# Performance work log

Measured on AMD Instinct MI355X. Metric: run time of the kernel, lower is better.

## Reference

```python
import jax, jax.numpy as jnp
import numpy as np

B, N, C = 32, 512, 256          # batch, proposals per scene, pooled feature dim
K = 16                          # knn neighbors
NN = B * N                      # total nodes = 16384
E = NN * K                      # total edges = 262144
L0_IN = 2 * C + 7               # EdgeConv layer-0 input (edge embedding appended)
EPS = 1e-5


def _xavier(key, fan_in, fan_out):
    s = float(np.sqrt(6.0 / (fan_in + fan_out)))
    return jax.random.uniform(key, (fan_in, fan_out), jnp.float32, -s, s)


def setup_inputs() -> dict:
    key = jax.random.key(0)
    ks = jax.random.split(key, 12)
    inp = {}
    inp["pooled_features"] = jax.random.normal(ks[0], (B, N, C), jnp.float32)
    inp["rois"] = jax.random.normal(ks[1], (B, N, 7), jnp.float32)
    inp["edge_src"] = jax.random.randint(ks[2], (E,), 0, NN)
    inp["edge_dst"] = jax.random.randint(ks[3], (E,), 0, NN)
    # global-info MLP: Linear(C+7 -> C) + BatchNorm(C) + ReLU
    inp["Wg"] = _xavier(ks[4], C + 7, C)
    inp["bg"] = jnp.zeros((C,), jnp.float32)
    inp["gg"] = jnp.ones((C,), jnp.float32)
    inp["betag"] = jnp.zeros((C,), jnp.float32)
    # EdgeConv 0: Linear(2C+7 -> C); EdgeConv 1,2: Linear(2C -> C)
    inp["W0"] = _xavier(ks[5], L0_IN, C)
    inp["b0"] = jnp.zeros((C,), jnp.float32)
    inp["g0"] = jnp.ones((C,), jnp.float32)
    inp["beta0"] = jnp.zeros((C,), jnp.float32)
    inp["W1"] = _xavier(ks[6], 2 * C, C)
    inp["b1"] = jnp.zeros((C,), jnp.float32)
    inp["g1"] = jnp.ones((C,), jnp.float32)
    inp["beta1"] = jnp.zeros((C,), jnp.float32)
    inp["W2"] = _xavier(ks[7], 2 * C, C)
    inp["b2"] = jnp.zeros((C,), jnp.float32)
    inp["g2"] = jnp.ones((C,), jnp.float32)
    inp["beta2"] = jnp.zeros((C,), jnp.float32)
    return inp


def _bn_relu(h, gamma, beta):
    # training-mode BatchNorm over the row (node/edge) dimension
    mu = jnp.mean(h, axis=0)
    var = jnp.mean(jnp.square(h - mu), axis=0)
    return jax.nn.relu((h - mu) * jax.lax.rsqrt(var + EPS) * gamma + beta)


def _edge_conv(x, src, dst, edge_attr, W, b, gamma, beta):
    x_j = x[src]          # source-node features  [E, D]
    x_i = x[dst]          # target-node features  [E, D]
    parts = [x_j - x_i, x_i]
    if edge_attr is not None:
        parts.append(edge_attr)
    m = jnp.concatenate(parts, axis=-1)          # [E, in_dim]
    h = _bn_relu(m @ W + b, gamma, beta)         # [E, C]
    out = jax.ops.segment_max(h, dst, num_segments=NN)  # scatter-max per target node
    return jnp.where(jnp.isneginf(out), 0.0, out)        # empty segments -> 0


def reference(pooled_features, rois, edge_src, edge_dst,
              Wg, bg, gg, betag,
              W0, b0, g0, beta0,
              W1, b1, g1, beta1,
              W2, b2, g2, beta2):
    boxes = rois.reshape(NN, 7)
    pf = pooled_features.reshape(NN, C)
    # global information MLP (CONCATENATED): cat(pooled, boxes) -> Linear+BN+ReLU
    x0 = _bn_relu(jnp.concatenate([pf, boxes], axis=-1) @ Wg + bg, gg, betag)
    # edge embedding: box delta from source to target
    edge_attr = boxes[edge_src] - boxes[edge_dst]
    x1 = _edge_conv(x0, edge_src, edge_dst, edge_attr, W0, b0, g0, beta0)
    x2 = _edge_conv(x1, edge_src, edge_dst, None, W1, b1, g1, beta1)
    x3 = _edge_conv(x2, edge_src, edge_dst, None, W2, b2, g2, beta2)
    return jnp.concatenate([x0, x1, x2, x3], axis=-1)  # related_features [NN, 4C]
```

## Files before the change

### kernel.cpp

```cpp
#include <hip/hip_runtime.h>
#include <hip/hip_bf16.h>
#include <hip/hip_fp16.h>
#include <math.h>
#include <stdint.h>


constexpr int NNODE = 16384;
constexpr int NEDGE = 262144;
constexpr int CD    = 256;
constexpr float EPSB = 1e-5f;

typedef __attribute__((ext_vector_type(8))) short bf16x8;
typedef __attribute__((ext_vector_type(8))) unsigned short u16x8;
typedef __attribute__((ext_vector_type(4))) float f32x4;
typedef __attribute__((ext_vector_type(4))) _Float16 h16x4;
typedef __attribute__((ext_vector_type(8))) _Float16 h16x8;

__device__ inline unsigned short bf_hi_rne(float f) {
  unsigned int u = __float_as_uint(f);
  u += 0x7fffu + ((u >> 16) & 1u);
  return (unsigned short)(u >> 16);
}

__global__ void build_wt(const float* __restrict__ W, const float* __restrict__ b,
                         unsigned short* __restrict__ Wth, unsigned short* __restrict__ Wtl,
                         int has_box) {
  int k = threadIdx.x;
  int n = blockIdx.x;
  if (k >= 288) return;
  float v = 0.0f;
  if (n < 256) {
    if (k < 256)      v = W[k * 256 + n];
    else if (k < 263) v = has_box ? W[(512 + (k - 256)) * 256 + n] : 0.0f;
  } else {
    int n2 = n - 256;
    if (k < 256)      v = W[(256 + k) * 256 + n2] - W[k * 256 + n2];
    else if (k < 263) v = has_box ? -W[(512 + (k - 256)) * 256 + n2] : 0.0f;
    else if (k == 263) v = b[n2];
  }
  unsigned short hi = bf_hi_rne(v);
  float fh = __uint_as_float((unsigned int)hi << 16);
  Wth[n * 288 + k] = hi;
  Wtl[n * 288 + k] = bf_hi_rne(v - fh);
}

__global__ void build_wtg(const float* __restrict__ Wg, const float* __restrict__ bg,
                          unsigned short* __restrict__ Wth, unsigned short* __restrict__ Wtl) {
  int k = threadIdx.x;
  int n = blockIdx.x;
  if (k >= 288) return;
  float v = 0.0f;
  if (k < 263)       v = Wg[k * 256 + n];
  else if (k == 263) v = bg[n];
  unsigned short hi = bf_hi_rne(v);
  float fh = __uint_as_float((unsigned int)hi << 16);
  Wth[n * 288 + k] = hi;
  Wtl[n * 288 + k] = bf_hi_rne(v - fh);
}

__global__ void build_boxf(const float* __restrict__ rois, float* __restrict__ boxf) {
  int n = blockIdx.x * 256 + threadIdx.x;
  float v[8];
#pragma unroll
  for (int j = 0; j < 7; j++) v[j] = rois[n * 7 + j];
  v[7] = 1.0f;
  *(float4*)(boxf + (size_t)n * 8)     = make_float4(v[0], v[1], v[2], v[3]);
  *(float4*)(boxf + (size_t)n * 8 + 4) = make_float4(v[4], v[5], v[6], v[7]);
}

__global__ void hist_kernel(const int* __restrict__ dst, int* __restrict__ counts) {
  int e = blockIdx.x * 256 + threadIdx.x;
  atomicAdd(&counts[dst[e]], 1);
}

__global__ __launch_bounds__(1024) void scan_kernel(const int* __restrict__ counts,
                                                    int* __restrict__ offsets,
                                                    int* __restrict__ cursor) {
  __shared__ int ssum[1024];
  int t = threadIdx.x;
  int base = t * 16;
  int loc[16];
  int s = 0;
#pragma unroll
  for (int i = 0; i < 16; i++) { loc[i] = s; s += counts[base + i]; }
  ssum[t] = s;
  __syncthreads();
  for (int off = 1; off < 1024; off <<= 1) {
    int v = (t >= off) ? ssum[t - off] : 0;
    __syncthreads();
    ssum[t] += v;
    __syncthreads();
  }
  int excl = (t > 0) ? ssum[t - 1] : 0;
#pragma unroll
  for (int i = 0; i < 16; i++) {
    int o = excl + loc[i];
    offsets[base + i] = o;
    cursor[base + i]  = o;
  }
  if (t == 1023) offsets[NNODE] = excl + s;
}

__global__ void scatter_kernel(const int* __restrict__ src, const int* __restrict__ dst,
                               int* __restrict__ cursor, int* __restrict__ csr_src) {
  int e = blockIdx.x * 256 + threadIdx.x;
  int p = atomicAdd(&cursor[dst[e]], 1);
  csr_src[p] = src[e];
}

__global__ __launch_bounds__(256) void gemm_mfma(
    const float* __restrict__ X, int xstride,
    const float* __restrict__ boxf,
    const unsigned short* __restrict__ Wth, const unsigned short* __restrict__ Wtl,
    float* __restrict__ out, int Nw, int half_out) {
  __shared__ alignas(16) char lds[4 * 8192];
  const int tid  = threadIdx.x;
  const int lane = tid & 63;
  const int wave = tid >> 6;
  const int wm = wave >> 1, wn = wave & 1;
  const int m0 = blockIdx.x * 128;
  const int n0 = blockIdx.y * 128;
  const int srow0 = tid >> 2;
  const int sc8   = tid & 3;

  f32x4 acc[4][4];
#pragma unroll
  for (int i = 0; i < 4; i++)
#pragma unroll
    for (int j = 0; j < 4; j++) acc[i][j] = (f32x4)0.0f;

  float a_f[2][8];
  u16x8 b_h[2], b_l[2];

  auto load_global = [&](int kt) {
#pragma unroll
    for (int p = 0; p < 2; p++) {
      int row = p * 64 + srow0;
      if (kt < 8) {
        const float* src = X + (size_t)(m0 + row) * xstride + kt * 32 + sc8 * 8;
        float4 v0 = *(const float4*)src;
        float4 v1 = *(const float4*)(src + 4);
        a_f[p][0] = v0.x; a_f[p][1] = v0.y; a_f[p][2] = v0.z; a_f[p][3] = v0.w;
        a_f[p][4] = v1.x; a_f[p][5] = v1.y; a_f[p][6] = v1.z; a_f[p][7] = v1.w;
      } else if (sc8 == 0) {
        float4 v0 = *(const float4*)(boxf + (size_t)(m0 + row) * 8);
        float4 v1 = *(const float4*)(boxf + (size_t)(m0 + row) * 8 + 4);
        a_f[p][0] = v0.x; a_f[p][1] = v0.y; a_f[p][2] = v0.z; a_f[p][3] = v0.w;
        a_f[p][4] = v1.x; a_f[p][5] = v1.y; a_f[p][6] = v1.z; a_f[p][7] = v1.w;
      } else {
#pragma unroll
        for (int j = 0; j < 8; j++) a_f[p][j] = 0.0f;
      }
      const size_t woff = (size_t)(n0 + row) * 288 + kt * 32 + sc8 * 8;
      b_h[p] = *(const u16x8*)(Wth + woff);
      b_l[p] = *(const u16x8*)(Wtl + woff);
    }
  };

  auto write_lds = [&]() {
#pragma unroll
    for (int p = 0; p < 2; p++) {
      int row = p * 64 + srow0;
      int off = row * 64 + 16 * sc8;
      u16x8 hi, lo;
#pragma unroll
      for (int j = 0; j < 8; j++) {
        float f = a_f[p][j];
        unsigned short h = bf_hi_rne(f);
        float fh = __uint_as_float((unsigned int)h << 16);
        hi[j] = h;
        lo[j] = bf_hi_rne(f - fh);
      }
      *(u16x8*)(lds + off)         = hi;
      *(u16x8*)(lds + 8192 + off)  = lo;
      *(u16x8*)(lds + 16384 + off) = b_h[p];
      *(u16x8*)(lds + 24576 + off) = b_l[p];
    }
  };

  load_global(0);
  const int kblk = lane >> 4;
  for (int kt = 0; kt < 9; kt++) {
    __syncthreads();
    write_lds();
    __syncthreads();
    if (kt < 8) load_global(kt + 1);

    bf16x8 ah[4], al[4];
#pragma unroll
    for (int i = 0; i < 4; i++) {
      int fm = wm * 64 + i * 16 + (lane & 15);
      int off = fm * 64 + 16 * kblk;
      ah[i] = *(const bf16x8*)(lds + off);
      al[i] = *(const bf16x8*)(lds + 8192 + off);
    }
#pragma unroll
    for (int j = 0; j < 4; j++) {
      int fn = wn * 64 + j * 16 + (lane & 15);
      int off = fn * 64 + 16 * kblk;
      bf16x8 bh = *(const bf16x8*)(lds + 16384 + off);
      bf16x8 bl = *(const bf16x8*)(lds + 24576 + off);
#pragma unroll
      for (int i = 0; i < 4; i++) {
        acc[i][j] = __builtin_amdgcn_mfma_f32_16x16x32_bf16(bh, ah[i], acc[i][j], 0, 0, 0);
        acc[i][j] = __builtin_amdgcn_mfma_f32_16x16x32_bf16(bh, al[i], acc[i][j], 0, 0, 0);
        acc[i][j] = __builtin_amdgcn_mfma_f32_16x16x32_bf16(bl, ah[i], acc[i][j], 0, 0, 0);
      }
    }
  }
#pragma unroll
  for (int i = 0; i < 4; i++) {
    int m = m0 + wm * 64 + i * 16 + (lane & 15);
#pragma unroll
    for (int j = 0; j < 4; j++) {
      int n = n0 + wn * 64 + j * 16 + (lane >> 4) * 4;
      if (half_out) {
        h16x4 o;
        o[0] = (_Float16)acc[i][j].x; o[1] = (_Float16)acc[i][j].y;
        o[2] = (_Float16)acc[i][j].z; o[3] = (_Float16)acc[i][j].w;
        *(h16x4*)((_Float16*)out + (size_t)m * Nw + n) = o;
      } else {
        *(f32x4*)(out + (size_t)m * Nw + n) = acc[i][j];
      }
    }
  }
}

constexpr int EPB = 8;
__global__ __launch_bounds__(256) void edge_pass(
    const _Float16* __restrict__ PQ,
    const int* __restrict__ offsets, const int* __restrict__ csr_src,
    float* __restrict__ M, float* __restrict__ psum, float* __restrict__ psq) {
  __shared__ float red[2][4][256];
  const int tid = threadIdx.x;
  const int wave = tid >> 6, lane = tid & 63;
  const int h = lane >> 5, li = lane & 31;
  const int c8 = li * 8;
  float sum[8] = {}, sq[8] = {};

  for (int nn = 0; nn < 2; nn++) {
    const int d = blockIdx.x * EPB + wave * 2 + nn;
    const int beg = offsets[d], end = offsets[d + 1];
    if (beg >= end) continue;
    h16x8 qv = *(const h16x8*)(PQ + (size_t)d * 512 + 256 + c8);
    float qf[8], mx[8];
#pragma unroll
    for (int j = 0; j < 8; j++) { qf[j] = (float)qv[j]; mx[j] = -INFINITY; }

    for (int e = beg; e < end; e += 8) {
      int idx[4];
      bool full = (e + 8 <= end);
      if (full) {
#pragma unroll
        for (int i = 0; i < 4; i++) idx[i] = csr_src[e + 2 * i + h];
        h16x8 pv[4];
#pragma unroll
        for (int i = 0; i < 4; i++)
          pv[i] = *(const h16x8*)(PQ + (size_t)idx[i] * 512 + c8);
#pragma unroll
        for (int i = 0; i < 4; i++)
#pragma unroll
          for (int j = 0; j < 8; j++) {
            float hh = (float)pv[i][j] + qf[j];
            mx[j] = fmaxf(mx[j], hh);
            sum[j] += hh;
            sq[j] = fmaf(hh, hh, sq[j]);
          }
      } else {
        bool live[4];
#pragma unroll
        for (int i = 0; i < 4; i++) {
          int ei = e + 2 * i + h;
          live[i] = ei < end;
          idx[i] = csr_src[live[i] ? ei : end - 1];
        }
        h16x8 pv[4];
#pragma unroll
        for (int i = 0; i < 4; i++)
          pv[i] = *(const h16x8*)(PQ + (size_t)idx[i] * 512 + c8);
#pragma unroll
        for (int i = 0; i < 4; i++)
#pragma unroll
          for (int j = 0; j < 8; j++) {
            float hh = (float)pv[i][j] + qf[j];
            mx[j] = fmaxf(mx[j], hh);
            float z = live[i] ? hh : 0.0f;
            sum[j] += z;
            sq[j] = fmaf(z, z, sq[j]);
          }
      }
    }
#pragma unroll
    for (int j = 0; j < 8; j++)
      mx[j] = fmaxf(mx[j], __shfl_xor(mx[j], 32));
    float4 o = (h == 0) ? make_float4(mx[0], mx[1], mx[2], mx[3])
                        : make_float4(mx[4], mx[5], mx[6], mx[7]);
    *(float4*)(M + (size_t)d * 256 + c8 + h * 4) = o;
  }

#pragma unroll
  for (int j = 0; j < 8; j++) {
    sum[j] += __shfl_xor(sum[j], 32);
    sq[j]  += __shfl_xor(sq[j], 32);
  }
  if (h == 0) {
    float4 s0 = make_float4(sum[0], sum[1], sum[2], sum[3]);
    float4 s1 = make_float4(sum[4], sum[5], sum[6], sum[7]);
    float4 q0 = make_float4(sq[0], sq[1], sq[2], sq[3]);
    float4 q1 = make_float4(sq[4], sq[5], sq[6], sq[7]);
    *(float4*)&red[0][wave][c8]     = s0;
    *(float4*)&red[0][wave][c8 + 4] = s1;
    *(float4*)&red[1][wave][c8]     = q0;
    *(float4*)&red[1][wave][c8 + 4] = q1;
  }
  __syncthreads();
  int c = tid;
  float ts = red[0][0][c] + red[0][1][c] + red[0][2][c] + red[0][3][c];
  float tq = red[1][0][c] + red[1][1][c] + red[1][2][c] + red[1][3][c];
  atomicAdd(&psum[c], ts);
  atomicAdd(&psq[c], tq);
}

__global__ void stats_dense(const float* __restrict__ H,
                            float* __restrict__ psum, float* __restrict__ psq) {
  int c  = threadIdx.x;
  int r0 = blockIdx.x * 16;
  float sum = 0.f, sq = 0.f;
  for (int r = r0; r < r0 + 16; r++) {
    float h = H[r * CD + c];
    sum += h;
    sq  += h * h;
  }
  atomicAdd(&psum[c], sum);
  atomicAdd(&psq[c], sq);
}

__global__ void finalize_stats(const float* __restrict__ psum, const float* __restrict__ psq,
                               float invcount, float* __restrict__ mu, float* __restrict__ rstd) {
  int c = threadIdx.x;
  float m = psum[c] * invcount;
  float v = psq[c] * invcount - m * m;
  v = fmaxf(v, 0.0f);
  mu[c]   = m;
  rstd[c] = 1.0f / sqrtf(v + EPSB);
}

__global__ void normalize_write(const float* __restrict__ H, const int* __restrict__ counts,
                                const float* __restrict__ mu, const float* __restrict__ rstd,
                                const float* __restrict__ gamma, const float* __restrict__ beta,
                                float* __restrict__ out, int col0) {
  int c  = threadIdx.x;
  int n0 = blockIdx.x * 8;
  float mc = mu[c], rc = rstd[c], gc = gamma[c], bc = beta[c];
  for (int n = n0; n < n0 + 8; n++) {
    float v = 0.0f;
    if (!counts || counts[n] != 0) {
      float h = H[n * CD + c];
      v = fmaxf((h - mc) * rc * gc + bc, 0.0f);
    }
    out[n * 1024 + col0 + c] = v;
  }
}

extern "C" void kernel_launch(void* const* d_in, const int* in_sizes, int n_in,
                              void* d_out, int out_size, void* d_ws, size_t ws_size,
                              hipStream_t stream) {
  const float* pf    = (const float*)d_in[0];
  const float* rois  = (const float*)d_in[1];
  const int*   esrc  = (const int*)d_in[2];
  const int*   edst  = (const int*)d_in[3];
  const float* Wg    = (const float*)d_in[4];
  const float* bg    = (const float*)d_in[5];
  const float* gg    = (const float*)d_in[6];
  const float* betag = (const float*)d_in[7];
  const float* Wl[3]  = {(const float*)d_in[8],  (const float*)d_in[12], (const float*)d_in[16]};
  const float* bl[3]  = {(const float*)d_in[9],  (const float*)d_in[13], (const float*)d_in[17]};
  const float* gl[3]  = {(const float*)d_in[10], (const float*)d_in[14], (const float*)d_in[18]};
  const float* bel[3] = {(const float*)d_in[11], (const float*)d_in[15], (const float*)d_in[19]};
  float* out = (float*)d_out;

  float* ws    = (float*)d_ws;
  _Float16* PQ = (_Float16*)ws;
  float* Mbuf  = ws + (size_t)NNODE * 256;
  float* psum  = Mbuf + (size_t)NNODE * CD;
  float* psq   = psum + CD;
  float* mu    = psq + CD;
  float* rstd  = mu + CD;
  float* boxf  = rstd + CD;
  unsigned short* wt = (unsigned short*)(boxf + (size_t)NNODE * 8);
  unsigned short* wtg_h = wt + 3 * 2 * 512 * 288;
  unsigned short* wtg_l = wtg_h + 256 * 288;
  int* counts  = (int*)(wtg_l + 256 * 288);
  int* offsets = counts + NNODE;
  int* cursor  = offsets + NNODE + 1;
  int* csr     = cursor + NNODE;

  hipMemsetAsync(counts, 0, NNODE * sizeof(int), stream);
  build_boxf<<<NNODE / 256, 256, 0, stream>>>(rois, boxf);
  build_wtg<<<256, 320, 0, stream>>>(Wg, bg, wtg_h, wtg_l);
  for (int l = 0; l < 3; l++)
    build_wt<<<512, 320, 0, stream>>>(Wl[l], bl[l],
                                      wt + l * 2 * 512 * 288,
                                      wt + l * 2 * 512 * 288 + 512 * 288,
                                      l == 0 ? 1 : 0);
  hist_kernel<<<NEDGE / 256, 256, 0, stream>>>(edst, counts);
  scan_kernel<<<1, 1024, 0, stream>>>(counts, offsets, cursor);
  scatter_kernel<<<NEDGE / 256, 256, 0, stream>>>(esrc, edst, cursor, csr);

  hipMemsetAsync(psum, 0, 2 * CD * sizeof(float), stream);
  {
    dim3 g(NNODE / 128, 256 / 128);
    gemm_mfma<<<g, 256, 0, stream>>>(pf, CD, boxf, wtg_h, wtg_l, Mbuf, CD, 0);
  }
  stats_dense<<<NNODE / 16, 256, 0, stream>>>(Mbuf, psum, psq);
  finalize_stats<<<1, 256, 0, stream>>>(psum, psq, 1.0f / NNODE, mu, rstd);
  normalize_write<<<NNODE / 8, 256, 0, stream>>>(Mbuf, nullptr, mu, rstd, gg, betag, out, 0);

  for (int l = 0; l < 3; l++) {
    dim3 g(NNODE / 128, 512 / 128);
    gemm_mfma<<<g, 256, 0, stream>>>(out + l * CD, 1024, boxf,
                                     wt + l * 2 * 512 * 288,
                                     wt + l * 2 * 512 * 288 + 512 * 288,
                                     (float*)PQ, 512, 1);
    hipMemsetAsync(psum, 0, 2 * CD * sizeof(float), stream);
    edge_pass<<<NNODE / EPB, 256, 0, stream>>>(PQ, offsets, csr, Mbuf, psum, psq);
    finalize_stats<<<1, 256, 0, stream>>>(psum, psq, 1.0f / NEDGE, mu, rstd);
    normalize_write<<<NNODE / 8, 256, 0, stream>>>(Mbuf, counts, mu, rstd, gl[l], bel[l],
                                                   out, (l + 1) * CD);
  }
}
```

Measured before the change: 504.0 us.

## Pre-split GEMM inputs to bf16 hi/lo and load tiles via global_load_lds

```diff
diff --git a/kernel.cpp b/kernel.cpp
--- a/kernel.cpp
+++ b/kernel.cpp
@@ -20,6 +20,12 @@
   unsigned int u = __float_as_uint(f);
   u += 0x7fffu + ((u >> 16) & 1u);
   return (unsigned short)(u >> 16);
+}
+
+__device__ __forceinline__ void gload16(const void* g, void* l) {
+  __builtin_amdgcn_global_load_lds(
+      (__attribute__((address_space(1))) void*)(void*)g,
+      (__attribute__((address_space(3))) void*)l, 16, 0, 0);
 }
 
 __global__ void build_wt(const float* __restrict__ W, const float* __restrict__ b,
@@ -58,14 +64,42 @@
   Wtl[n * 288 + k] = bf_hi_rne(v - fh);
 }
 
-__global__ void build_boxf(const float* __restrict__ rois, float* __restrict__ boxf) {
+__global__ void build_boxf16(const float* __restrict__ rois,
+                             unsigned short* __restrict__ hi, unsigned short* __restrict__ lo) {
   int n = blockIdx.x * 256 + threadIdx.x;
-  float v[8];
-#pragma unroll
-  for (int j = 0; j < 7; j++) v[j] = rois[n * 7 + j];
-  v[7] = 1.0f;
-  *(float4*)(boxf + (size_t)n * 8)     = make_float4(v[0], v[1], v[2], v[3]);
-  *(float4*)(boxf + (size_t)n * 8 + 4) = make_float4(v[4], v[5], v[6], v[7]);
+  u16x8 h8 = (u16x8)0, l8 = (u16x8)0;
+#pragma unroll
+  for (int j = 0; j < 8; j++) {
+    float v = (j < 7) ? rois[n * 7 + j] : 1.0f;
+    unsigned short h = bf_hi_rne(v);
+    h8[j] = h;
+    l8[j] = bf_hi_rne(v - __uint_as_float((unsigned int)h << 16));
+  }
+  *(u16x8*)(hi + (size_t)n * 32) = h8;
+  *(u16x8*)(lo + (size_t)n * 32) = l8;
+  u16x8 z = (u16x8)0;
+#pragma unroll
+  for (int c = 1; c < 4; c++) {
+    *(u16x8*)(hi + (size_t)n * 32 + c * 8) = z;
+    *(u16x8*)(lo + (size_t)n * 32 + c * 8) = z;
+  }
+}
+
+__global__ void convert_split(const float* __restrict__ src,
+                              unsigned short* __restrict__ hi, unsigned short* __restrict__ lo) {
+  size_t i0 = ((size_t)blockIdx.x * 256 + threadIdx.x) * 8;
+  float4 a = *(const float4*)(src + i0);
+  float4 b = *(const float4*)(src + i0 + 4);
+  float v[8] = {a.x, a.y, a.z, a.w, b.x, b.y, b.z, b.w};
+  u16x8 h8, l8;
+#pragma unroll
+  for (int j = 0; j < 8; j++) {
+    unsigned short h = bf_hi_rne(v[j]);
+    h8[j] = h;
+    l8[j] = bf_hi_rne(v[j] - __uint_as_float((unsigned int)h << 16));
+  }
+  *(u16x8*)(hi + i0) = h8;
+  *(u16x8*)(lo + i0) = l8;
 }
 
 __global__ void hist_kernel(const int* __restrict__ dst, int* __restrict__ counts) {
@@ -109,8 +143,8 @@
 }
 
 __global__ __launch_bounds__(256) void gemm_mfma(
-    const float* __restrict__ X, int xstride,
-    const float* __restrict__ boxf,
+    const unsigned short* __restrict__ Ah, const unsigned short* __restrict__ Al,
+    const unsigned short* __restrict__ bxh, const unsigned short* __restrict__ bxl,
     const unsigned short* __restrict__ Wth, const unsigned short* __restrict__ Wtl,
     float* __restrict__ out, int Nw, int half_out) {
   __shared__ alignas(16) char lds[4 * 8192];
@@ -120,8 +154,8 @@
   const int wm = wave >> 1, wn = wave & 1;
   const int m0 = blockIdx.x * 128;
   const int n0 = blockIdx.y * 128;
-  const int srow0 = tid >> 2;
-  const int sc8   = tid & 3;
+  const int srow = tid >> 2;
+  const int sc8  = (tid & 3) * 8;
 
   f32x4 acc[4][4];
 #pragma unroll
@@ -129,62 +163,27 @@
 #pragma unroll
     for (int j = 0; j < 4; j++) acc[i][j] = (f32x4)0.0f;
 
-  float a_f[2][8];
-  u16x8 b_h[2], b_l[2];
-
-  auto load_global = [&](int kt) {
-#pragma unroll
-    for (int p = 0; p < 2; p++) {
-      int row = p * 64 + srow0;
-      if (kt < 8) {
-        const float* src = X + (size_t)(m0 + row) * xstride + kt * 32 + sc8 * 8;
-        float4 v0 = *(const float4*)src;
-        float4 v1 = *(const float4*)(src + 4);
-        a_f[p][0] = v0.x; a_f[p][1] = v0.y; a_f[p][2] = v0.z; a_f[p][3] = v0.w;
-        a_f[p][4] = v1.x; a_f[p][5] = v1.y; a_f[p][6] = v1.z; a_f[p][7] = v1.w;
-      } else if (sc8 == 0) {
-        float4 v0 = *(const float4*)(boxf + (size_t)(m0 + row) * 8);
-        float4 v1 = *(const float4*)(boxf + (size_t)(m0 + row) * 8 + 4);
-        a_f[p][0] = v0.x; a_f[p][1] = v0.y; a_f[p][2] = v0.z; a_f[p][3] = v0.w;
-        a_f[p][4] = v1.x; a_f[p][5] = v1.y; a_f[p][6] = v1.z; a_f[p][7] = v1.w;
-      } else {
-#pragma unroll
-        for (int j = 0; j < 8; j++) a_f[p][j] = 0.0f;
-      }
-      const size_t woff = (size_t)(n0 + row) * 288 + kt * 32 + sc8 * 8;
-      b_h[p] = *(const u16x8*)(Wth + woff);
-      b_l[p] = *(const u16x8*)(Wtl + woff);
-    }
-  };
-
-  auto write_lds = [&]() {
-#pragma unroll
-    for (int p = 0; p < 2; p++) {
-      int row = p * 64 + srow0;
-      int off = row * 64 + 16 * sc8;
-      u16x8 hi, lo;
-#pragma unroll
-      for (int j = 0; j < 8; j++) {
-        float f = a_f[p][j];
-        unsigned short h = bf_hi_rne(f);
-        float fh = __uint_as_float((unsigned int)h << 16);
-        hi[j] = h;
-        lo[j] = bf_hi_rne(f - fh);
-      }
-      *(u16x8*)(lds + off)         = hi;
-      *(u16x8*)(lds + 8192 + off)  = lo;
-      *(u16x8*)(lds + 16384 + off) = b_h[p];
-      *(u16x8*)(lds + 24576 + off) = b_l[p];
-    }
-  };
-
-  load_global(0);
   const int kblk = lane >> 4;
   for (int kt = 0; kt < 9; kt++) {
+    if (kt) __syncthreads();
+#pragma unroll
+    for (int p = 0; p < 2; p++) {
+      int row = p * 64 + srow;
+      const unsigned short *gah, *gal;
+      if (kt < 8) {
+        size_t o = (size_t)(m0 + row) * 256 + kt * 32 + sc8;
+        gah = Ah + o; gal = Al + o;
+      } else {
+        size_t o = (size_t)(m0 + row) * 32 + sc8;
+        gah = bxh + o; gal = bxl + o;
+      }
+      gload16(gah, lds + p * 4096 + tid * 16);
+      gload16(gal, lds + 8192 + p * 4096 + tid * 16);
+      size_t wo = (size_t)(n0 + row) * 288 + kt * 32 + sc8;
+      gload16(Wth + wo, lds + 16384 + p * 4096 + tid * 16);
+      gload16(Wtl + wo, lds + 24576 + p * 4096 + tid * 16);
+    }
     __syncthreads();
-    write_lds();
-    __syncthreads();
-    if (kt < 8) load_global(kt + 1);
 
     bf16x8 ah[4], al[4];
 #pragma unroll
@@ -238,65 +237,94 @@
   const int c8 = li * 8;
   float sum[8] = {}, sq[8] = {};
 
-  for (int nn = 0; nn < 2; nn++) {
-    const int d = blockIdx.x * EPB + wave * 2 + nn;
-    const int beg = offsets[d], end = offsets[d + 1];
-    if (beg >= end) continue;
-    h16x8 qv = *(const h16x8*)(PQ + (size_t)d * 512 + 256 + c8);
-    float qf[8], mx[8];
-#pragma unroll
-    for (int j = 0; j < 8; j++) { qf[j] = (float)qv[j]; mx[j] = -INFINITY; }
-
-    for (int e = beg; e < end; e += 8) {
-      int idx[4];
-      bool full = (e + 8 <= end);
-      if (full) {
-#pragma unroll
-        for (int i = 0; i < 4; i++) idx[i] = csr_src[e + 2 * i + h];
-        h16x8 pv[4];
-#pragma unroll
-        for (int i = 0; i < 4; i++)
-          pv[i] = *(const h16x8*)(PQ + (size_t)idx[i] * 512 + c8);
-#pragma unroll
-        for (int i = 0; i < 4; i++)
-#pragma unroll
-          for (int j = 0; j < 8; j++) {
-            float hh = (float)pv[i][j] + qf[j];
-            mx[j] = fmaxf(mx[j], hh);
-            sum[j] += hh;
-            sq[j] = fmaf(hh, hh, sq[j]);
-          }
-      } else {
-        bool live[4];
-#pragma unroll
-        for (int i = 0; i < 4; i++) {
-          int ei = e + 2 * i + h;
-          live[i] = ei < end;
-          idx[i] = csr_src[live[i] ? ei : end - 1];
-        }
-        h16x8 pv[4];
-#pragma unroll
-        for (int i = 0; i < 4; i++)
-          pv[i] = *(const h16x8*)(PQ + (size_t)idx[i] * 512 + c8);
-#pragma unroll
-        for (int i = 0; i < 4; i++)
-#pragma unroll
-          for (int j = 0; j < 8; j++) {
-            float hh = (float)pv[i][j] + qf[j];
-            mx[j] = fmaxf(mx[j], hh);
-            float z = live[i] ? hh : 0.0f;
-            sum[j] += z;
-            sq[j] = fmaf(z, z, sq[j]);
-          }
+  const int d0 = blockIdx.x * EPB + wave * 2;
+  const int d1 = d0 + 1;
+  int e0 = offsets[d0];
+  const int end0 = offsets[d0 + 1];
+  int e1 = offsets[d1];
+  const int end1 = offsets[d1 + 1];
+
+  h16x8 q0v = *(const h16x8*)(PQ + (size_t)d0 * 512 + 256 + c8);
+  h16x8 q1v = *(const h16x8*)(PQ + (size_t)d1 * 512 + 256 + c8);
+  float q0[8], q1[8], mx0[8], mx1[8];
+#pragma unroll
+  for (int j = 0; j < 8; j++) {
+    q0[j] = (float)q0v[j]; q1[j] = (float)q1v[j];
+    mx0[j] = -INFINITY;    mx1[j] = -INFINITY;
+  }
+
+  while (e0 < end0 || e1 < end1) {
+    const bool a0 = e0 < end0, a1 = e1 < end1;
+    int i0[4], i1[4];
+    if (a0) {
+#pragma unroll
+      for (int i = 0; i < 4; i++) {
+        int ei = e0 + 2 * i + h;
+        i0[i] = csr_src[ei < end0 ? ei : end0 - 1];
       }
     }
-#pragma unroll
-    for (int j = 0; j < 8; j++)
-      mx[j] = fmaxf(mx[j], __shfl_xor(mx[j], 32));
-    float4 o = (h == 0) ? make_float4(mx[0], mx[1], mx[2], mx[3])
-                        : make_float4(mx[4], mx[5], mx[6], mx[7]);
-    *(float4*)(M + (size_t)d * 256 + c8 + h * 4) = o;
-  }
+    if (a1) {
+#pragma unroll
+      for (int i = 0; i < 4; i++) {
+        int ei = e1 + 2 * i + h;
+        i1[i] = csr_src[ei < end1 ? ei : end1 - 1];
+      }
+    }
+    h16x8 p0[4], p1[4];
+    if (a0) {
+#pragma unroll
+      for (int i = 0; i < 4; i++)
+        p0[i] = *(const h16x8*)(PQ + (size_t)i0[i] * 512 + c8);
+    }
+    if (a1) {
+#pragma unroll
+      for (int i = 0; i < 4; i++)
+        p1[i] = *(const h16x8*)(PQ + (size_t)i1[i] * 512 + c8);
+    }
+
+#define PROC_NODE(P, Q, MX, EE, END)                                        \
+    {                                                                       \
+      const int nl = (END) - (EE);                                          \
+      if (nl >= 8) {                                                        \
+        _Pragma("unroll")                                                   \
+        for (int i = 0; i < 4; i++)                                         \
+          _Pragma("unroll")                                                 \
+          for (int j = 0; j < 8; j++) {                                     \
+            float hh = (float)P[i][j] + Q[j];                               \
+            MX[j] = fmaxf(MX[j], hh);                                       \
+            sum[j] += hh; sq[j] = fmaf(hh, hh, sq[j]);                      \
+          }                                                                 \
+      } else {                                                              \
+        _Pragma("unroll")                                                   \
+        for (int i = 0; i < 4; i++) {                                       \
+          const bool live = (2 * i + h) < nl;                               \
+          _Pragma("unroll")                                                 \
+          for (int j = 0; j < 8; j++) {                                     \
+            float hh = (float)P[i][j] + Q[j];                               \
+            MX[j] = fmaxf(MX[j], hh);                                       \
+            float z = live ? hh : 0.f;                                      \
+            sum[j] += z; sq[j] = fmaf(z, z, sq[j]);                         \
+          }                                                                 \
+        }                                                                   \
+      }                                                                     \
+    }
+
+    if (a0) { PROC_NODE(p0, q0, mx0, e0, end0); e0 += 8; }
+    if (a1) { PROC_NODE(p1, q1, mx1, e1, end1); e1 += 8; }
+#undef PROC_NODE
+  }
+
+#pragma unroll
+  for (int j = 0; j < 8; j++) {
+    mx0[j] = fmaxf(mx0[j], __shfl_xor(mx0[j], 32));
+    mx1[j] = fmaxf(mx1[j], __shfl_xor(mx1[j], 32));
+  }
+  float4 o0 = (h == 0) ? make_float4(mx0[0], mx0[1], mx0[2], mx0[3])
+                       : make_float4(mx0[4], mx0[5], mx0[6], mx0[7]);
+  float4 o1 = (h == 0) ? make_float4(mx1[0], mx1[1], mx1[2], mx1[3])
+                       : make_float4(mx1[4], mx1[5], mx1[6], mx1[7]);
+  *(float4*)(M + (size_t)d0 * 256 + c8 + h * 4) = o0;
+  *(float4*)(M + (size_t)d1 * 256 + c8 + h * 4) = o1;
 
 #pragma unroll
   for (int j = 0; j < 8; j++) {
@@ -304,14 +332,10 @@
     sq[j]  += __shfl_xor(sq[j], 32);
   }
   if (h == 0) {
-    float4 s0 = make_float4(sum[0], sum[1], sum[2], sum[3]);
-    float4 s1 = make_float4(sum[4], sum[5], sum[6], sum[7]);
-    float4 q0 = make_float4(sq[0], sq[1], sq[2], sq[3]);
-    float4 q1 = make_float4(sq[4], sq[5], sq[6], sq[7]);
-    *(float4*)&red[0][wave][c8]     = s0;
-    *(float4*)&red[0][wave][c8 + 4] = s1;
-    *(float4*)&red[1][wave][c8]     = q0;
-    *(float4*)&red[1][wave][c8 + 4] = q1;
+    *(float4*)&red[0][wave][c8]     = make_float4(sum[0], sum[1], sum[2], sum[3]);
+    *(float4*)&red[0][wave][c8 + 4] = make_float4(sum[4], sum[5], sum[6], sum[7]);
+    *(float4*)&red[1][wave][c8]     = make_float4(sq[0], sq[1], sq[2], sq[3]);
+    *(float4*)&red[1][wave][c8 + 4] = make_float4(sq[4], sq[5], sq[6], sq[7]);
   }
   __syncthreads();
   int c = tid;
@@ -348,7 +372,8 @@
 __global__ void normalize_write(const float* __restrict__ H, const int* __restrict__ counts,
                                 const float* __restrict__ mu, const float* __restrict__ rstd,
                                 const float* __restrict__ gamma, const float* __restrict__ beta,
-                                float* __restrict__ out, int col0) {
+                                float* __restrict__ out, int col0,
+                                unsigned short* __restrict__ xh, unsigned short* __restrict__ xl) {
   int c  = threadIdx.x;
   int n0 = blockIdx.x * 8;
   float mc = mu[c], rc = rstd[c], gc = gamma[c], bc = beta[c];
@@ -359,6 +384,11 @@
       v = fmaxf((h - mc) * rc * gc + bc, 0.0f);
     }
     out[n * 1024 + col0 + c] = v;
+    if (xh) {
+      unsigned short hv = bf_hi_rne(v);
+      xh[(size_t)n * 256 + c] = hv;
+      xl[(size_t)n * 256 + c] = bf_hi_rne(v - __uint_as_float((unsigned int)hv << 16));
+    }
   }
 }
 
@@ -386,8 +416,11 @@
   float* psq   = psum + CD;
   float* mu    = psq + CD;
   float* rstd  = mu + CD;
-  float* boxf  = rstd + CD;
-  unsigned short* wt = (unsigned short*)(boxf + (size_t)NNODE * 8);
+  unsigned short* Ah = (unsigned short*)(rstd + CD);
+  unsigned short* Al = Ah + (size_t)NNODE * 256;
+  unsigned short* bxh = Al + (size_t)NNODE * 256;
+  unsigned short* bxl = bxh + (size_t)NNODE * 32;
+  unsigned short* wt  = bxl + (size_t)NNODE * 32;
   unsigned short* wtg_h = wt + 3 * 2 * 512 * 288;
   unsigned short* wtg_l = wtg_h + 256 * 288;
   int* counts  = (int*)(wtg_l + 256 * 288);
@@ -396,7 +429,8 @@
   int* csr     = cursor + NNODE;
 
   hipMemsetAsync(counts, 0, NNODE * sizeof(int), stream);
-  build_boxf<<<NNODE / 256, 256, 0, stream>>>(rois, boxf);
+  build_boxf16<<<NNODE / 256, 256, 0, stream>>>(rois, bxh, bxl);
+  convert_split<<<NNODE * CD / (256 * 8), 256, 0, stream>>>(pf, Ah, Al);
   build_wtg<<<256, 320, 0, stream>>>(Wg, bg, wtg_h, wtg_l);
   for (int l = 0; l < 3; l++)
     build_wt<<<512, 320, 0, stream>>>(Wl[l], bl[l],
@@ -409,16 +443,17 @@
 
   hipMemsetAsync(psum, 0, 2 * CD * sizeof(float), stream);
   {
-    dim3 g(NNODE / 128, 256 / 128);
-    gemm_mfma<<<g, 256, 0, stream>>>(pf, CD, boxf, wtg_h, wtg_l, Mbuf, CD, 0);
+    dim3 g(NNODE / 128, 2);
+    gemm_mfma<<<g, 256, 0, stream>>>(Ah, Al, bxh, bxl, wtg_h, wtg_l, Mbuf, 256, 0);
   }
   stats_dense<<<NNODE / 16, 256, 0, stream>>>(Mbuf, psum, psq);
   finalize_stats<<<1, 256, 0, stream>>>(psum, psq, 1.0f / NNODE, mu, rstd);
-  normalize_write<<<NNODE / 8, 256, 0, stream>>>(Mbuf, nullptr, mu, rstd, gg, betag, out, 0);
+  normalize_write<<<NNODE / 8, 256, 0, stream>>>(Mbuf, nullptr, mu, rstd, gg, betag,
+                                                 out, 0, Ah, Al);
 
   for (int l = 0; l < 3; l++) {
-    dim3 g(NNODE / 128, 512 / 128);
-    gemm_mfma<<<g, 256, 0, stream>>>(out + l * CD, 1024, boxf,
+    dim3 g(NNODE / 128, 4);
+    gemm_mfma<<<g, 256, 0, stream>>>(Ah, Al, bxh, bxl,
                                      wt + l * 2 * 512 * 288,
                                      wt + l * 2 * 512 * 288 + 512 * 288,
                                      (float*)PQ, 512, 1);
@@ -426,6 +461,8 @@
     edge_pass<<<NNODE / EPB, 256, 0, stream>>>(PQ, offsets, csr, Mbuf, psum, psq);
     finalize_stats<<<1, 256, 0, stream>>>(psum, psq, 1.0f / NEDGE, mu, rstd);
     normalize_write<<<NNODE / 8, 256, 0, stream>>>(Mbuf, counts, mu, rstd, gl[l], bel[l],
-                                                   out, (l + 1) * CD);
-  }
-}
+                                                   out, (l + 1) * CD,
+                                                   l < 2 ? Ah : nullptr,
+                                                   l < 2 ? Al : nullptr);
+  }
+}
```

Measured after the change: 495.2 us. About the same (-1.7%).
